# Performance work log

Hardware: AMD Instinct MI355X
Metric: run time of the kernel (lower is better)

## Reference

```python
import jax, jax.numpy as jnp
import numpy as np

B = 65536
H = 128          # hidden_size
IN_BOT = 128     # input_bottom_size
IN_TOP = 128     # input_top_size
GATE_W = 4 * H + 1  # 513: 4 gate chunks + 1 boundary logit
HARD_A = 1.0
ROUND_TH = 0.5


def setup_inputs() -> dict:
    key = jax.random.key(0)
    ks = jax.random.split(key, 10)
    sd = 1.0 / np.sqrt(H)
    return {
        "h_bottom": jax.random.normal(ks[0], (B, IN_BOT), jnp.float32),
        "h":        jax.random.normal(ks[1], (B, H), jnp.float32),
        "h_top":    jax.random.normal(ks[2], (B, IN_TOP), jnp.float32),
        "c":        jax.random.normal(ks[3], (B, H), jnp.float32),
        "z":        jax.random.randint(ks[4], (B, 1), 0, 2).astype(jnp.float32),
        "z_bottom": jax.random.randint(ks[5], (B, 1), 0, 2).astype(jnp.float32),
        "W": jax.random.uniform(ks[6], (IN_BOT, GATE_W), jnp.float32, -sd, sd),
        "R": jax.random.uniform(ks[7], (H, GATE_W), jnp.float32, -sd, sd),
        "U": jax.random.uniform(ks[8], (IN_TOP, GATE_W), jnp.float32, -sd, sd),
        "b": jax.random.uniform(ks[9], (GATE_W,), jnp.float32, -sd, sd),
    }


def _hard_sigm(x, a=HARD_A):
    # HardSigm: clip((a*x + 1)/2, 0, 1)
    return jnp.clip((a * x + 1.0) * 0.5, 0.0, 1.0)


def _round_st(z_tilde, th=ROUND_TH):
    # threshold rounding with straight-through gradient (identity backward)
    hard = (z_tilde > th).astype(z_tilde.dtype)
    return z_tilde + jax.lax.stop_gradient(hard - z_tilde)


def reference(h_bottom, h, h_top, c, z, z_bottom, W, R, U, b):
    # fused gate pre-activations: [B, 4H+1]
    s = (h_bottom * z_bottom) @ W + h @ R + (h_top * z) @ U + b
    si = s[:, 0 * H:1 * H]
    sg = s[:, 1 * H:2 * H]
    so = s[:, 2 * H:3 * H]
    sf = s[:, 3 * H:4 * H]
    sz = s[:, 4 * H:4 * H + 1]
    i = jax.nn.sigmoid(si)
    g = jnp.tanh(sg)
    o = jax.nn.sigmoid(so)
    f = jax.nn.sigmoid(sf)
    ig = i * g
    # FLUSH if z==1; COPY if z==0 & z_bottom==0; UPDATE otherwise
    c_new = jnp.where(z == 1.0, ig, jnp.where(z_bottom == 0.0, c, c * f + ig))
    h_new = jnp.where((z == 0.0) & (z_bottom == 0.0), h, jnp.tanh(c_new) * o)
    z_new = _round_st(_hard_sigm(sz))
    return (h_new, c_new, z_new)
```

## Files before the change

### kernel.cpp

```cpp
#include <hip/hip_runtime.h>
#include <hip/hip_bf16.h>


#define MT   128
#define BK   32
#define NKC  12
#define NT   512
#define COFF 8388608
#define ZOFF 16777216

using short8 = __attribute__((ext_vector_type(8))) short;
using f32x4  = __attribute__((ext_vector_type(4))) float;

__device__ __forceinline__ unsigned short f2bf(float f) {
  union { float f; unsigned u; } v; v.f = f;
  unsigned r = (v.u + 0x7FFFu + ((v.u >> 16) & 1u)) >> 16;
  return (unsigned short)r;
}

__device__ __forceinline__ void async_copy16(const void* g, void* l) {
  __builtin_amdgcn_global_load_lds(
      (const __attribute__((address_space(1))) unsigned int*)g,
      (__attribute__((address_space(3))) unsigned int*)l, 16, 0, 0);
}

__device__ __forceinline__ float sigm(float x)     { return 1.f / (1.f + __expf(-x)); }
__device__ __forceinline__ float tanh_fast(float x){ return 1.f - 2.f / (1.f + __expf(2.f * x)); }

__global__ void prep_weights(const float* __restrict__ W, const float* __restrict__ R,
                             const float* __restrict__ U, unsigned short* __restrict__ Wt) {
  int idx = blockIdx.x * blockDim.x + threadIdx.x;
  if (idx >= NKC * 512 * 4) return;
  int up = idx & 3;
  int n  = (idx >> 2) & 511;
  int c  = idx >> 11;
  int ul = up ^ ((n >> 1) & 3);
  int k0 = c * 32 + ul * 8;
  const float* src; int kb;
  if (k0 < 128)      { src = W; kb = 0;   }
  else if (k0 < 256) { src = R; kb = 128; }
  else               { src = U; kb = 256; }
  const float* colp = src + (size_t)(k0 - kb) * 513 + n;
  unsigned short vs[8];
  #pragma unroll
  for (int j = 0; j < 8; ++j) vs[j] = f2bf(colp[j * 513]);
  uint4 o;
  o.x = (unsigned)vs[0] | ((unsigned)vs[1] << 16);
  o.y = (unsigned)vs[2] | ((unsigned)vs[3] << 16);
  o.z = (unsigned)vs[4] | ((unsigned)vs[5] << 16);
  o.w = (unsigned)vs[6] | ((unsigned)vs[7] << 16);
  reinterpret_cast<uint4*>(Wt)[idx] = o;
}

__global__ __launch_bounds__(512, 2)
void hmlstm_main(const float* __restrict__ hb, const float* __restrict__ hs,
                 const float* __restrict__ ht, const float* __restrict__ cs,
                 const float* __restrict__ zp, const float* __restrict__ zbp,
                 const float* __restrict__ W,  const float* __restrict__ R,
                 const float* __restrict__ U,  const float* __restrict__ b,
                 const unsigned short* __restrict__ Wt, float* __restrict__ out)
{
  __shared__ unsigned short ldsW[512 * BK];
  __shared__ unsigned short ldsA[2][MT * BK];
  __shared__ float  ldsWL[384];
  __shared__ double ldsSZ[NT];

  const int tid  = threadIdx.x;
  const int l    = tid & 63;
  const int wv   = tid >> 6;
  const int ws   = wv & 3;
  const int wr   = wv >> 2;
  const int q    = l >> 4;
  const int lr   = l & 15;
  const int row0 = blockIdx.x * MT;

  for (int k = tid; k < 384; k += NT) {
    ldsWL[k] = (k < 128) ? W[k * 513 + 512]
             : (k < 256) ? R[(k - 128) * 513 + 512]
                         : U[(k - 256) * 513 + 512];
  }

  const int m    = tid >> 2;
  const int p    = tid & 3;
  const int arow = row0 + m;
  const float zbv = zbp[arow];
  const float zv  = zp[arow];
  double szacc = 0.0;

  f32x4 acc[4][8];
  {
    f32x4 zf = {0.f, 0.f, 0.f, 0.f};
    #pragma unroll
    for (int i = 0; i < 4; ++i)
      #pragma unroll
      for (int j = 0; j < 8; ++j) acc[i][j] = zf;
  }

  const int aW = m * BK + ((p ^ ((m >> 1) & 3)) * 8);

  __syncthreads();

  auto stageA = [&](int kc, int buf) {
    const float* src  = (kc < 4) ? hb : (kc < 8) ? hs : ht;
    const float scale = (kc < 4) ? zbv : (kc < 8) ? 1.f : zv;
    const float* sp = src + (size_t)arow * 128 + (kc & 3) * 32 + p * 8;
    f32x4 v0 = *(const f32x4*)sp;
    f32x4 v1 = *(const f32x4*)(sp + 4);
    v0 *= scale; v1 *= scale;
    const float* wl = ldsWL + kc * 32 + p * 8;
    szacc += (double)v0.x * wl[0] + (double)v0.y * wl[1]
           + (double)v0.z * wl[2] + (double)v0.w * wl[3]
           + (double)v1.x * wl[4] + (double)v1.y * wl[5]
           + (double)v1.z * wl[6] + (double)v1.w * wl[7];
    uint4 pk;
    pk.x = (unsigned)f2bf(v0.x) | ((unsigned)f2bf(v0.y) << 16);
    pk.y = (unsigned)f2bf(v0.z) | ((unsigned)f2bf(v0.w) << 16);
    pk.z = (unsigned)f2bf(v1.x) | ((unsigned)f2bf(v1.y) << 16);
    pk.w = (unsigned)f2bf(v1.z) | ((unsigned)f2bf(v1.w) << 16);
    *(uint4*)&ldsA[buf][aW] = pk;
  };

  stageA(0, 0);

  for (int kc = 0; kc < NKC; ++kc) {
    const int cur = kc & 1, nxt = cur ^ 1;
    const unsigned short* gW = Wt + kc * (512 * BK);
    #pragma unroll
    for (int r = 0; r < 4; ++r) {
      int eo = (wv * 4 + r) * 512;
      async_copy16(gW + eo + l * 8, ldsW + eo);
    }
    if (kc < NKC - 1) stageA(kc + 1, nxt);
    __syncthreads();

    short8 bfr[8];
    #pragma unroll
    for (int tn = 0; tn < 8; ++tn) {
      int nc = (tn >> 1) * 128 + ws * 32 + (tn & 1) * 16 + lr;
      bfr[tn] = *(const short8*)&ldsW[nc * BK + ((q ^ ((nc >> 1) & 3)) * 8)];
    }
    #pragma unroll
    for (int s = 0; s < 4; ++s) {
      int mr = wr * 64 + s * 16 + lr;
      short8 af = *(const short8*)&ldsA[cur][mr * BK + ((q ^ ((mr >> 1) & 3)) * 8)];
      #pragma unroll
      for (int tn = 0; tn < 8; ++tn)
        acc[s][tn] = __builtin_amdgcn_mfma_f32_16x16x32_bf16(af, bfr[tn], acc[s][tn], 0, 0, 0);
    }
    __syncthreads();
  }

  ldsSZ[tid] = szacc;
  __syncthreads();
  if (tid < MT) {
    double ss = ldsSZ[tid * 4] + ldsSZ[tid * 4 + 1] + ldsSZ[tid * 4 + 2] + ldsSZ[tid * 4 + 3];
    float s = (float)ss + b[512];
    out[ZOFF + row0 + tid] = (s > 0.f) ? 1.f : 0.f;
  }

  float bias[2][4];
  #pragma unroll
  for (int th = 0; th < 2; ++th) {
    const int col = ws * 32 + th * 16 + lr;
    bias[th][0] = b[col];       bias[th][1] = b[128 + col];
    bias[th][2] = b[256 + col]; bias[th][3] = b[384 + col];
  }
  #pragma unroll
  for (int s = 0; s < 4; ++s) {
    #pragma unroll
    for (int r = 0; r < 4; ++r) {
      const int row = row0 + wr * 64 + s * 16 + q * 4 + r;
      const float zr  = zp[row];
      const float zbr = zbp[row];
      const size_t rowoff = (size_t)row * 128;
      #pragma unroll
      for (int th = 0; th < 2; ++th) {
        const int col = ws * 32 + th * 16 + lr;
        const size_t off = rowoff + col;
        float si = acc[s][0 + th][r] + bias[th][0];
        float sg = acc[s][2 + th][r] + bias[th][1];
        float so = acc[s][4 + th][r] + bias[th][2];
        float sf = acc[s][6 + th][r] + bias[th][3];
        float iv = sigm(si);
        float gv = tanh_fast(sg);
        float ov = sigm(so);
        float fv = sigm(sf);
        float ig = iv * gv;
        float cv = cs[off];
        float hv = hs[off];
        float cn = (zr == 1.f) ? ig : ((zbr == 0.f) ? cv : cv * fv + ig);
        float hn = (zr == 0.f && zbr == 0.f) ? hv : tanh_fast(cn) * ov;
        out[off]        = hn;
        out[COFF + off] = cn;
      }
    }
  }
}

extern "C" void kernel_launch(void* const* d_in, const int* in_sizes, int n_in,
                              void* d_out, int out_size, void* d_ws, size_t ws_size,
                              hipStream_t stream) {
  const float* hb  = (const float*)d_in[0];
  const float* hs  = (const float*)d_in[1];
  const float* ht  = (const float*)d_in[2];
  const float* cs  = (const float*)d_in[3];
  const float* zp  = (const float*)d_in[4];
  const float* zbp = (const float*)d_in[5];
  const float* W   = (const float*)d_in[6];
  const float* R   = (const float*)d_in[7];
  const float* U   = (const float*)d_in[8];
  const float* b   = (const float*)d_in[9];
  unsigned short* Wt = (unsigned short*)d_ws;
  float* out = (float*)d_out;

  prep_weights<<<dim3(96), dim3(256), 0, stream>>>(W, R, U, Wt);
  hmlstm_main<<<dim3(65536 / MT), dim3(NT), 0, stream>>>(
      hb, hs, ht, cs, zp, zbp, W, R, U, b, Wt, out);
}
```

Measured before the change: 251.7 us.

## Double-buffer weights and stage fp32 activations into LDS via async global-to-LDS copies

The main loop now double-buffers both the weight tile and the activation tile, using async global_load_lds copies for activations too (raw fp32, XOR-swizzled). Scaling by z and the bf16 conversion move to fragment-load time. Explicit waitcnt and s_barrier replace the two __syncthreads per K step. The boundary-logit dot product is now computed from LDS and reduced with shuffles instead of a shared double array. The prep kernel transposes through LDS for coalesced reads and also writes the boundary column weights. The aim is to overlap global loads with MFMA work and cut register staging. The cost is doubled LDS use, which may lower occupancy, and the hand-coded waitcnt values are fragile.

```diff
diff --git a/kernel.cpp b/kernel.cpp
--- a/kernel.cpp
+++ b/kernel.cpp
@@ -6,6 +6,8 @@
 #define BK   32
 #define NKC  12
 #define NT   512
+#define WCH  (512*BK)
+#define ACH  (MT*BK)
 #define COFF 8388608
 #define ZOFF 16777216
 
@@ -18,6 +20,11 @@
   return (unsigned short)r;
 }
 
+__device__ __forceinline__ unsigned pk_bf2(float x, float y) {
+  union { float f; unsigned u; } a, b; a.f = x; b.f = y;
+  return __builtin_amdgcn_perm(b.u + 0x8000u, a.u + 0x8000u, 0x07060302u);
+}
+
 __device__ __forceinline__ void async_copy16(const void* g, void* l) {
   __builtin_amdgcn_global_load_lds(
       (const __attribute__((address_space(1))) unsigned int*)g,
@@ -27,43 +34,57 @@
 __device__ __forceinline__ float sigm(float x)     { return 1.f / (1.f + __expf(-x)); }
 __device__ __forceinline__ float tanh_fast(float x){ return 1.f - 2.f / (1.f + __expf(2.f * x)); }
 
-__global__ void prep_weights(const float* __restrict__ W, const float* __restrict__ R,
-                             const float* __restrict__ U, unsigned short* __restrict__ Wt) {
-  int idx = blockIdx.x * blockDim.x + threadIdx.x;
-  if (idx >= NKC * 512 * 4) return;
-  int up = idx & 3;
-  int n  = (idx >> 2) & 511;
-  int c  = idx >> 11;
-  int ul = up ^ ((n >> 1) & 3);
-  int k0 = c * 32 + ul * 8;
-  const float* src; int kb;
-  if (k0 < 128)      { src = W; kb = 0;   }
-  else if (k0 < 256) { src = R; kb = 128; }
-  else               { src = U; kb = 256; }
-  const float* colp = src + (size_t)(k0 - kb) * 513 + n;
-  unsigned short vs[8];
-  #pragma unroll
-  for (int j = 0; j < 8; ++j) vs[j] = f2bf(colp[j * 513]);
-  uint4 o;
-  o.x = (unsigned)vs[0] | ((unsigned)vs[1] << 16);
-  o.y = (unsigned)vs[2] | ((unsigned)vs[3] << 16);
-  o.z = (unsigned)vs[4] | ((unsigned)vs[5] << 16);
-  o.w = (unsigned)vs[6] | ((unsigned)vs[7] << 16);
-  reinterpret_cast<uint4*>(Wt)[idx] = o;
+__global__ __launch_bounds__(256)
+void prep_weights(const float* __restrict__ W, const float* __restrict__ R,
+                  const float* __restrict__ U, unsigned short* __restrict__ Wt,
+                  float* __restrict__ WL) {
+  __shared__ unsigned short T[32][136];
+  const int c = blockIdx.x >> 2, g = blockIdx.x & 3, tid = threadIdx.x;
+  const int n0 = g * 128, k0 = c * 32;
+  #pragma unroll 4
+  for (int it = 0; it < 16; ++it) {
+    int r = it * 2 + (tid >> 7);
+    int k = k0 + r;
+    const float* row = (k < 128) ? W + (size_t)k * 513
+                     : (k < 256) ? R + (size_t)(k - 128) * 513
+                                 : U + (size_t)(k - 256) * 513;
+    T[r][tid & 127] = f2bf(row[n0 + (tid & 127)]);
+  }
+  if (g == 0 && tid < 32) {
+    int k = k0 + tid;
+    const float* row = (k < 128) ? W + (size_t)k * 513
+                     : (k < 256) ? R + (size_t)(k - 128) * 513
+                                 : U + (size_t)(k - 256) * 513;
+    WL[k] = row[512];
+  }
+  __syncthreads();
+  for (int t = tid; t < 512; t += 256) {
+    int nl = t >> 2, u = t & 3;
+    int n  = n0 + nl;
+    int kl = (u ^ ((n >> 1) & 3)) * 8;
+    unsigned short vs[8];
+    #pragma unroll
+    for (int j = 0; j < 8; ++j) vs[j] = T[kl + j][nl];
+    uint4 o;
+    o.x = (unsigned)vs[0] | ((unsigned)vs[1] << 16);
+    o.y = (unsigned)vs[2] | ((unsigned)vs[3] << 16);
+    o.z = (unsigned)vs[4] | ((unsigned)vs[5] << 16);
+    o.w = (unsigned)vs[6] | ((unsigned)vs[7] << 16);
+    reinterpret_cast<uint4*>(Wt)[(size_t)c * 2048 + (size_t)n * 4 + u] = o;
+  }
 }
 
 __global__ __launch_bounds__(512, 2)
 void hmlstm_main(const float* __restrict__ hb, const float* __restrict__ hs,
                  const float* __restrict__ ht, const float* __restrict__ cs,
                  const float* __restrict__ zp, const float* __restrict__ zbp,
-                 const float* __restrict__ W,  const float* __restrict__ R,
-                 const float* __restrict__ U,  const float* __restrict__ b,
-                 const unsigned short* __restrict__ Wt, float* __restrict__ out)
+                 const float* __restrict__ b,
+                 const unsigned short* __restrict__ Wt,
+                 const float* __restrict__ WLg, float* __restrict__ out)
 {
-  __shared__ unsigned short ldsW[512 * BK];
-  __shared__ unsigned short ldsA[2][MT * BK];
-  __shared__ float  ldsWL[384];
-  __shared__ double ldsSZ[NT];
+  __shared__ unsigned short ldsW[2][WCH];
+  __shared__ float ldsA[2][ACH];
+  __shared__ float ldsWL[384];
 
   const int tid  = threadIdx.x;
   const int l    = tid & 63;
@@ -74,17 +95,17 @@
   const int lr   = l & 15;
   const int row0 = blockIdx.x * MT;
 
-  for (int k = tid; k < 384; k += NT) {
-    ldsWL[k] = (k < 128) ? W[k * 513 + 512]
-             : (k < 256) ? R[(k - 128) * 513 + 512]
-                         : U[(k - 256) * 513 + 512];
-  }
-
-  const int m    = tid >> 2;
-  const int p    = tid & 3;
-  const int arow = row0 + m;
-  const float zbv = zbp[arow];
-  const float zv  = zp[arow];
+  if (tid < 384) ldsWL[tid] = WLg[tid];
+
+  float zrow[4], zbrow[4];
+  #pragma unroll
+  for (int s = 0; s < 4; ++s) {
+    int r = row0 + wr * 64 + s * 16 + lr;
+    zrow[s] = zp[r]; zbrow[s] = zbp[r];
+  }
+  const int rsz = wv * 16 + (l >> 2);
+  const float z_sz  = zp[row0 + rsz];
+  const float zb_sz = zbp[row0 + rsz];
   double szacc = 0.0;
 
   f32x4 acc[4][8];
@@ -96,66 +117,84 @@
       for (int j = 0; j < 8; ++j) acc[i][j] = zf;
   }
 
-  const int aW = m * BK + ((p ^ ((m >> 1) & 3)) * 8);
-
-  __syncthreads();
-
-  auto stageA = [&](int kc, int buf) {
-    const float* src  = (kc < 4) ? hb : (kc < 8) ? hs : ht;
-    const float scale = (kc < 4) ? zbv : (kc < 8) ? 1.f : zv;
-    const float* sp = src + (size_t)arow * 128 + (kc & 3) * 32 + p * 8;
-    f32x4 v0 = *(const f32x4*)sp;
-    f32x4 v1 = *(const f32x4*)(sp + 4);
-    v0 *= scale; v1 *= scale;
-    const float* wl = ldsWL + kc * 32 + p * 8;
-    szacc += (double)v0.x * wl[0] + (double)v0.y * wl[1]
-           + (double)v0.z * wl[2] + (double)v0.w * wl[3]
-           + (double)v1.x * wl[4] + (double)v1.y * wl[5]
-           + (double)v1.z * wl[6] + (double)v1.w * wl[7];
-    uint4 pk;
-    pk.x = (unsigned)f2bf(v0.x) | ((unsigned)f2bf(v0.y) << 16);
-    pk.y = (unsigned)f2bf(v0.z) | ((unsigned)f2bf(v0.w) << 16);
-    pk.z = (unsigned)f2bf(v1.x) | ((unsigned)f2bf(v1.y) << 16);
-    pk.w = (unsigned)f2bf(v1.z) | ((unsigned)f2bf(v1.w) << 16);
-    *(uint4*)&ldsA[buf][aW] = pk;
-  };
-
-  stageA(0, 0);
-
-  for (int kc = 0; kc < NKC; ++kc) {
-    const int cur = kc & 1, nxt = cur ^ 1;
-    const unsigned short* gW = Wt + kc * (512 * BK);
+  auto stageW = [&](int c, int buf) {
+    const unsigned short* gW = Wt + (size_t)c * WCH;
     #pragma unroll
     for (int r = 0; r < 4; ++r) {
       int eo = (wv * 4 + r) * 512;
-      async_copy16(gW + eo + l * 8, ldsW + eo);
-    }
-    if (kc < NKC - 1) stageA(kc + 1, nxt);
-    __syncthreads();
+      async_copy16(gW + eo + l * 8, &ldsW[buf][eo]);
+    }
+  };
+  auto stageA = [&](int c, int buf) {
+    const float* src = (c < 4) ? hb : (c < 8) ? hs : ht;
+    const int co = (c & 3) * 32;
+    #pragma unroll
+    for (int r = 0; r < 2; ++r) {
+      int U0 = (wv * 2 + r) * 64;
+      int m  = (U0 + l) >> 3;
+      int ul = ((U0 + l) & 7) ^ (m & 7);
+      async_copy16(src + (size_t)(row0 + m) * 128 + co + ul * 4,
+                   &ldsA[buf][U0 * 4]);
+    }
+  };
+
+  stageW(0, 0); stageA(0, 0);
+
+  #pragma unroll
+  for (int kc = 0; kc < NKC; ++kc) {
+    const int cur = kc & 1;
+    if (kc < NKC - 1) { stageW(kc + 1, cur ^ 1); stageA(kc + 1, cur ^ 1); }
+    __builtin_amdgcn_sched_barrier(0);
+    if (kc < NKC - 1) __builtin_amdgcn_s_waitcnt(0x0076);
+    else              __builtin_amdgcn_s_waitcnt(0x0070);
+    __builtin_amdgcn_s_barrier();
+    __builtin_amdgcn_sched_barrier(0);
 
     short8 bfr[8];
     #pragma unroll
     for (int tn = 0; tn < 8; ++tn) {
       int nc = (tn >> 1) * 128 + ws * 32 + (tn & 1) * 16 + lr;
-      bfr[tn] = *(const short8*)&ldsW[nc * BK + ((q ^ ((nc >> 1) & 3)) * 8)];
-    }
+      bfr[tn] = *(const short8*)&ldsW[cur][nc * BK + ((q ^ ((nc >> 1) & 3)) * 8)];
+    }
+    const float scm = (kc < 4) ? 0.f : (kc < 8) ? 1.f : 2.f;
     #pragma unroll
     for (int s = 0; s < 4; ++s) {
-      int mr = wr * 64 + s * 16 + lr;
-      short8 af = *(const short8*)&ldsA[cur][mr * BK + ((q ^ ((mr >> 1) & 3)) * 8)];
+      int m = wr * 64 + s * 16 + lr;
+      const float sc = (kc < 4) ? zbrow[s] : (kc < 8) ? 1.f : zrow[s];
+      f32x4 a0 = *(const f32x4*)&ldsA[cur][m * 32 + (((q * 2)     ^ (m & 7)) * 4)];
+      f32x4 a1 = *(const f32x4*)&ldsA[cur][m * 32 + (((q * 2 + 1) ^ (m & 7)) * 4)];
+      a0 *= sc; a1 *= sc;
+      short8 af;
+      ((unsigned*)&af)[0] = pk_bf2(a0.x, a0.y);
+      ((unsigned*)&af)[1] = pk_bf2(a0.z, a0.w);
+      ((unsigned*)&af)[2] = pk_bf2(a1.x, a1.y);
+      ((unsigned*)&af)[3] = pk_bf2(a1.z, a1.w);
       #pragma unroll
       for (int tn = 0; tn < 8; ++tn)
         acc[s][tn] = __builtin_amdgcn_mfma_f32_16x16x32_bf16(af, bfr[tn], acc[s][tn], 0, 0, 0);
     }
-    __syncthreads();
-  }
-
-  ldsSZ[tid] = szacc;
-  __syncthreads();
-  if (tid < MT) {
-    double ss = ldsSZ[tid * 4] + ldsSZ[tid * 4 + 1] + ldsSZ[tid * 4 + 2] + ldsSZ[tid * 4 + 3];
-    float s = (float)ss + b[512];
-    out[ZOFF + row0 + tid] = (s > 0.f) ? 1.f : 0.f;
+    {
+      int kq = (l & 3) * 2;
+      f32x4 s0 = *(const f32x4*)&ldsA[cur][rsz * 32 + ((kq       ^ (rsz & 7)) * 4)];
+      f32x4 s1 = *(const f32x4*)&ldsA[cur][rsz * 32 + (((kq + 1) ^ (rsz & 7)) * 4)];
+      const float* wl = &ldsWL[kc * 32 + (l & 3) * 8];
+      double d = (double)s0.x * wl[0] + (double)s0.y * wl[1]
+               + (double)s0.z * wl[2] + (double)s0.w * wl[3]
+               + (double)s1.x * wl[4] + (double)s1.y * wl[5]
+               + (double)s1.z * wl[6] + (double)s1.w * wl[7];
+      const float scz = (kc < 4) ? zb_sz : (kc < 8) ? 1.f : z_sz;
+      szacc += (double)scz * d;
+      (void)scm;
+    }
+    __builtin_amdgcn_sched_barrier(0);
+    __builtin_amdgcn_s_barrier();
+  }
+
+  szacc += __shfl_xor(szacc, 1);
+  szacc += __shfl_xor(szacc, 2);
+  if ((l & 3) == 0) {
+    float s = (float)(szacc + (double)b[512]);
+    out[ZOFF + row0 + rsz] = (s > 0.f) ? 1.f : 0.f;
   }
 
   float bias[2][4];
@@ -211,9 +250,10 @@
   const float* U   = (const float*)d_in[8];
   const float* b   = (const float*)d_in[9];
   unsigned short* Wt = (unsigned short*)d_ws;
+  float* WL = (float*)(Wt + (size_t)NKC * WCH);
   float* out = (float*)d_out;
 
-  prep_weights<<<dim3(96), dim3(256), 0, stream>>>(W, R, U, Wt);
+  prep_weights<<<dim3(48), dim3(256), 0, stream>>>(W, R, U, Wt, WL);
   hmlstm_main<<<dim3(65536 / MT), dim3(NT), 0, stream>>>(
-      hb, hs, ht, cs, zp, zbp, W, R, U, b, Wt, out);
-}
+      hb, hs, ht, cs, zp, zbp, b, Wt, WL, out);
+}
```

Result: slower. 256.9 us (+2.1%).
